# Kernel tuning notes

Measured on AMD Instinct MI355X. Metric: run time of the kernel, lower is better.

The kernel has to match this reference:

```python
import jax, jax.numpy as jnp
import numpy as np
from jax import lax

N, HW = 64, 240
C0, C1, C2, C3 = 3, 32, 64, 128
HEAD = 1280


def _conv(x, w, stride, pad):
    return lax.conv_general_dilated(
        x, w, (stride, stride), [(pad, pad), (pad, pad)],
        dimension_numbers=("NCHW", "OIHW", "NCHW"))


def _cbr(x, w, alpha, beta, stride, pad, do_relu=True):
    # conv2d with pre-folded BN: y = conv(x,w)*alpha + beta, then ReLU
    y = _conv(x, w, stride, pad)
    y = y * alpha[None, :, None, None] + beta[None, :, None, None]
    return jnp.maximum(y, 0.0) if do_relu else y


def setup_inputs() -> dict:
    key = jax.random.key(0)
    ks = jax.random.split(key, 13)
    f32 = jnp.float32
    inp = {
        "x": jax.random.normal(ks[0], (N, C0, HW, HW), dtype=f32),
        # stem 3x3 s2: 3 -> 32
        "w_stem": jax.random.normal(ks[1], (C1, C0, 3, 3), dtype=f32) * 0.1,
        "a_stem": jax.random.uniform(ks[2], (C1,), dtype=f32, minval=0.5, maxval=1.5),
        "b_stem": jax.random.normal(ks[3], (C1,), dtype=f32) * 0.1,
        # mid 3x3 s2: 32 -> 64
        "w1": jax.random.normal(ks[4], (C2, C1, 3, 3), dtype=f32) * 0.05,
        "a1": jax.random.uniform(ks[5], (C2,), dtype=f32, minval=0.5, maxval=1.5),
        "b1": jax.random.normal(ks[6], (C2,), dtype=f32) * 0.1,
        # pointwise 1x1 s1: 64 -> 128
        "w2": jax.random.normal(ks[7], (C3, C2, 1, 1), dtype=f32) * 0.05,
        "a2": jax.random.uniform(ks[8], (C3,), dtype=f32, minval=0.5, maxval=1.5),
        "b2": jax.random.normal(ks[9], (C3,), dtype=f32) * 0.1,
        # head: GAP + GEMV (w2d [Cout, Cin]) + BN-fold + ReLU
        "w_head": jax.random.normal(ks[10], (HEAD, C3), dtype=f32) * 0.05,
        "a_head": jax.random.uniform(ks[11], (HEAD,), dtype=f32, minval=0.5, maxval=1.5),
        "b_head": jax.random.normal(ks[12], (HEAD,), dtype=f32) * 0.1,
    }
    return inp


def reference(x, w_stem, a_stem, b_stem, w1, a1, b1, w2, a2, b2,
              w_head, a_head, b_head):
    h = _cbr(x, w_stem, a_stem, b_stem, stride=2, pad=1)   # [N,32,120,120]
    h = _cbr(h, w1, a1, b1, stride=2, pad=1)               # [N,64,60,60]
    h = _cbr(h, w2, a2, b2, stride=1, pad=0)               # [N,128,60,60]
    # head: global average pool + GEMV + folded-BN affine + ReLU
    gap = h.mean(axis=(2, 3))                              # [N,128]
    out = jnp.einsum("nc,oc->no", gap, w_head)             # [N,1280]
    out = out * a_head[None, :] + b_head[None, :]
    return jnp.maximum(out, 0.0)
```

## Files before the change

kernel.cpp:

```cpp
#include <hip/hip_runtime.h>

#define N_    64
#define HW_   240
#define H1_   120
#define H2_   60
#define C0_   3
#define C1_   32
#define C2_   64
#define C3_   128
#define HEAD_ 1280

typedef unsigned short US;
typedef short bf16x8 __attribute__((ext_vector_type(8)));
typedef float f32x16 __attribute__((ext_vector_type(16)));

__device__ __forceinline__ US f2bf(float f) {
  union { float f; unsigned u; } v; v.f = f;
  unsigned r = v.u + 0x7FFF + ((v.u >> 16) & 1);
  return (US)(r >> 16);
}

#define H1Q_ROW 3968
#define H1Q_PL  1984

#define ZCHN   368
#define ZTOT   (64 * ZCHN * 4)
__global__ __launch_bounds__(256) void k0_prep(
    const float* __restrict__ w1, const float* __restrict__ w2,
    const float* __restrict__ w0,
    US* __restrict__ h1q, US* __restrict__ wt1, US* __restrict__ wt2,
    US* __restrict__ wt0, float* __restrict__ gap) {
  int gid = blockIdx.x * 256 + threadIdx.x;
  if (gid < ZTOT) {
    int c = gid >> 2, q = gid & 3;
    int n = c / ZCHN, cc = c % ZCHN;
    long off; int y;
    if (cc < 124)      { y = 0;   off = (long)cc * 32; }
    else if (cc < 248) { y = 121; off = (long)(cc - 124) * 32; }
    else               { y = cc - 247; off = H1Q_PL; }
    uint4 z; z.x = z.y = z.z = z.w = 0u;
    *(uint4*)(h1q + ((long)(n * 122 + y)) * H1Q_ROW + off + q * 8) = z;
  } else if (gid < ZTOT + 18432) {
    int e = gid - ZTOT;
    int oc = e / 288, ic = (e / 9) % 32, ky = (e / 3) % 3, kx = e % 3;
    wt1[((ky * 3 + kx) * 64 + oc) * 32 + ic] = f2bf(w1[e]);
  } else if (gid < ZTOT + 18432 + 8192) {
    int e = gid - (ZTOT + 18432);
    wt2[e] = f2bf(w2[e]);
  } else if (gid < ZTOT + 18432 + 8192 + 1024) {
    int e = gid - (ZTOT + 18432 + 8192);
    int oc = e >> 5, k = e & 31;
    wt0[e] = (k < 27) ? f2bf(w0[oc * 27 + k]) : (US)0;
  } else if (gid < ZTOT + 18432 + 8192 + 1024 + 8192) {
    gap[gid - (ZTOT + 18432 + 8192 + 1024)] = 0.f;
  }
}

#define XSW 248
__global__ __launch_bounds__(256) void k1_mfma(
    const float* __restrict__ x, const US* __restrict__ wt0,
    const float* __restrict__ alpha, const float* __restrict__ beta,
    US* __restrict__ h1q) {
  __shared__ float xs[3 * 3 * XSW];
  __shared__ US ot[128 * 32];
  int y = blockIdx.x, n = blockIdx.y;
  int iy0 = 2 * y - 1;
  const float* xn = x + (long)n * C0_ * HW_ * HW_;
  for (int e = threadIdx.x; e < 540; e += 256) {
    int m = e % 60, seg = e / 60;
    int ic = seg / 3, r = seg % 3;
    int iy = iy0 + r;
    float4 v; v.x = v.y = v.z = v.w = 0.f;
    if (iy >= 0) v = *(const float4*)(xn + (long)ic * HW_ * HW_ + iy * HW_ + 4 * m);
    *(float4*)(xs + seg * XSW + 4 + 4 * m) = v;
  }
  if (threadIdx.x < 18) {
    int seg = threadIdx.x >> 1, end = threadIdx.x & 1;
    float4 z; z.x = z.y = z.z = z.w = 0.f;
    *(float4*)(xs + seg * XSW + (end ? 244 : 0)) = z;
  }
  __syncthreads();

  int t = threadIdx.x, wv = t >> 6, l = t & 63;
  int lane31 = l & 31, half = l >> 5;
  int ox = wv * 32 + lane31;
  int oxc = ox < H1_ ? ox : (H1_ - 1);

  float fa[16];
#pragma unroll
  for (int m = 0; m < 2; m++)
#pragma unroll
    for (int j = 0; j < 8; j++) {
      int k = m * 16 + half * 8 + j;
      float v = 0.f;
      if (k < 27) {
        int ic = k / 9, rem = k - ic * 9;
        int ky = rem / 3, kx = rem - ky * 3;
        v = xs[(ic * 3 + ky) * XSW + 3 + 2 * oxc + kx];
      }
      fa[m * 8 + j] = v;
    }
  bf16x8 a0, a1;
#pragma unroll
  for (int j = 0; j < 8; j++) {
    a0[j] = (short)f2bf(fa[j]);
    a1[j] = (short)f2bf(fa[8 + j]);
  }
  const US* wb = wt0 + lane31 * 32 + half * 8;
  bf16x8 b0 = *(const bf16x8*)(wb);
  bf16x8 b1 = *(const bf16x8*)(wb + 16);

  f32x16 acc;
#pragma unroll
  for (int i = 0; i < 16; i++) acc[i] = 0.f;
  acc = __builtin_amdgcn_mfma_f32_32x32x16_bf16(a0, b0, acc, 0, 0, 0);
  acc = __builtin_amdgcn_mfma_f32_32x32x16_bf16(a1, b1, acc, 0, 0, 0);

  int oc = lane31;
  float al = alpha[oc], be = beta[oc];
#pragma unroll
  for (int r = 0; r < 16; r++) {
    int row = (r & 3) + 8 * (r >> 2) + 4 * half;
    float v = fmaxf(fmaf(acc[r], al, be), 0.f);
    ot[(wv * 32 + row) * 32 + oc] = f2bf(v);
  }
  __syncthreads();

  long rowb = ((long)(n * 122 + y + 1)) * H1Q_ROW;
  for (int u = t; u < 480; u += 256) {
    int px = u >> 2, q = u & 3;
    int pl = px & 1;
    int m = (px + 1) >> 1;
    long addr = rowb + (pl ? H1Q_PL : 0) + (long)m * 32 + q * 8;
    *(uint4*)(h1q + addr) = *(const uint4*)(ot + px * 32 + q * 8);
  }
}

#define TS 72
__device__ __forceinline__ void gld_lds16(const void* g, void* l) {
  __builtin_amdgcn_global_load_lds(
      (const __attribute__((address_space(1))) unsigned int*)g,
      (__attribute__((address_space(3))) unsigned int*)l, 16, 0, 0);
}

__global__ __launch_bounds__(256) void k2_fused(
    const US* __restrict__ h1q, const US* __restrict__ wt1,
    const US* __restrict__ wt2,
    const float* __restrict__ a1, const float* __restrict__ b1,
    const float* __restrict__ a2, const float* __restrict__ b2,
    float* __restrict__ gap) {
  __shared__ __align__(16) US st[1536 * 8];
  __shared__ __align__(16) US tile[64 * TS];
  int t = threadIdx.x, w = t >> 6, l = t & 63;
  int lane31 = l & 31, half = l >> 5;

  int flat = blockIdx.y * 60 + blockIdx.x;
  int sf = (flat & 7) * 480 + (flat >> 3);
  int n = sf / 60, y = sf - n * 60;

  const US* src = h1q + ((long)(n * 122 + 2 * y)) * H1Q_ROW;
#pragma unroll
  for (int i = 0; i < 6; i++) {
    int b = (i * 256 + t) * 16;
    int sb = b ^ (((b >> 7) & 7) << 4);
    gld_lds16((const char*)src + sb, (char*)st + b);
  }
  __syncthreads();

  int wm = w & 1, wn = w >> 1;
  int px = wm * 32 + lane31;
  int xx = px < 60 ? px : 59;
  int oc = wn * 32 + lane31;
  int abase = xx * 32 + half * 8;

  f32x16 acc;
#pragma unroll
  for (int i = 0; i < 16; i++) acc[i] = 0.f;

#pragma unroll
  for (int ky = 0; ky < 3; ky++) {
#pragma unroll
    for (int kx = 0; kx < 3; kx++) {
      int aoff = ky * 3968 + (kx == 1 ? 0 : (kx == 0 ? 1984 : 2016)) + abase;
      const US* wk = wt1 + ((ky * 3 + kx) * 64 + oc) * 32 + half * 8;
#pragma unroll
      for (int c = 0; c < 2; c++) {
        int u = aoff + c * 16;
        int us = u ^ (((u >> 6) & 7) << 3);
        bf16x8 av = *(const bf16x8*)(st + us);
        bf16x8 bv = *(const bf16x8*)(wk + c * 16);
        acc = __builtin_amdgcn_mfma_f32_32x32x16_bf16(av, bv, acc, 0, 0, 0);
      }
    }
  }
  {
    float al = a1[oc], be = b1[oc];
#pragma unroll
    for (int r = 0; r < 16; r++) {
      int row = (r & 3) + 8 * (r >> 2) + 4 * half;
      tile[(wm * 32 + row) * TS + oc] = f2bf(fmaxf(fmaf(acc[r], al, be), 0.f));
    }
  }
  __syncthreads();

  int pt = w & 1;
  int og = w >> 1;
  const US* ab = tile + (pt * 32 + lane31) * TS + half * 8;
  bf16x8 af[4];
#pragma unroll
  for (int c = 0; c < 4; c++) af[c] = *(const bf16x8*)(ab + c * 16);

#pragma unroll
  for (int nt = 0; nt < 2; nt++) {
    int oc2 = (og * 2 + nt) * 32 + lane31;
    const US* bb = wt2 + oc2 * 64 + half * 8;
    f32x16 acc2;
#pragma unroll
    for (int i = 0; i < 16; i++) acc2[i] = 0.f;
#pragma unroll
    for (int c = 0; c < 4; c++) {
      bf16x8 bv = *(const bf16x8*)(bb + c * 16);
      acc2 = __builtin_amdgcn_mfma_f32_32x32x16_bf16(af[c], bv, acc2, 0, 0, 0);
    }
    float al2 = a2[oc2], be2 = b2[oc2];
    float s = 0.f;
    if (pt == 0) {
#pragma unroll
      for (int r = 0; r < 16; r++) s += fmaxf(fmaf(acc2[r], al2, be2), 0.f);
    } else {
#pragma unroll
      for (int r = 0; r < 16; r++) {
        int row = (r & 3) + 8 * (r >> 2) + 4 * half;
        if (32 + row < 60) s += fmaxf(fmaf(acc2[r], al2, be2), 0.f);
      }
    }
    s += __shfl_xor(s, 32);
    if (half == 0) atomicAdd(gap + n * C3_ + oc2, s);
  }
}

__global__ __launch_bounds__(256) void k4_head(
    const float* __restrict__ gap, const float* __restrict__ wh,
    const float* __restrict__ alpha, const float* __restrict__ beta,
    float* __restrict__ out) {
  __shared__ float g[C3_];
  int n = blockIdx.y;
  int o = blockIdx.x * 256 + threadIdx.x;
  if (threadIdx.x < C3_)
    g[threadIdx.x] = gap[n * C3_ + threadIdx.x] * (1.f / 3600.f);
  __syncthreads();
  const float* wr = wh + (long)o * C3_;
  float acc = 0.f;
#pragma unroll 8
  for (int c = 0; c < C3_; c += 4) {
    float4 wv = *(const float4*)(wr + c);
    acc = fmaf(wv.x, g[c],     acc);
    acc = fmaf(wv.y, g[c + 1], acc);
    acc = fmaf(wv.z, g[c + 2], acc);
    acc = fmaf(wv.w, g[c + 3], acc);
  }
  out[n * HEAD_ + o] = fmaxf(fmaf(acc, alpha[o], beta[o]), 0.f);
}

extern "C" void kernel_launch(void* const* d_in, const int* in_sizes, int n_in,
                              void* d_out, int out_size, void* d_ws,
                              size_t ws_size, hipStream_t stream) {
  const float* x      = (const float*)d_in[0];
  const float* w_stem = (const float*)d_in[1];
  const float* a_stem = (const float*)d_in[2];
  const float* b_stem = (const float*)d_in[3];
  const float* w1     = (const float*)d_in[4];
  const float* a1     = (const float*)d_in[5];
  const float* b1     = (const float*)d_in[6];
  const float* w2     = (const float*)d_in[7];
  const float* a2     = (const float*)d_in[8];
  const float* b2     = (const float*)d_in[9];
  const float* wh     = (const float*)d_in[10];
  const float* ah     = (const float*)d_in[11];
  const float* bh     = (const float*)d_in[12];
  float* out = (float*)d_out;

  US* h1q = (US*)d_ws;
  US* wt1 = h1q + (size_t)N_ * 122 * H1Q_ROW;
  US* wt2 = wt1 + 9 * 64 * 32;
  US* wt0 = wt2 + C3_ * C2_;
  float* gap = (float*)(wt0 + 1024);

  {
    int total = ZTOT + 18432 + 8192 + 1024 + 8192;
    k0_prep<<<(total + 255) / 256, 256, 0, stream>>>(w1, w2, w_stem, h1q,
                                                     wt1, wt2, wt0, gap);
  }
  {
    dim3 grid(H1_, N_);
    k1_mfma<<<grid, 256, 0, stream>>>(x, wt0, a_stem, b_stem, h1q);
  }
  {
    dim3 grid(H2_, N_);
    k2_fused<<<grid, 256, 0, stream>>>(h1q, wt1, wt2, a1, b1, a2, b2, gap);
  }
  {
    dim3 grid(HEAD_ / 256, N_);
    k4_head<<<grid, 256, 0, stream>>>(gap, wh, ah, bh, out);
  }
}
```

Baseline: 169.2 us.

## Make k2 blocks loop over output rows with ring-buffered input rows and register-resident weights

The fused conv kernel now gives each block a strip of 7-8 output rows of one image instead of a single row. Input rows sit in a 6-row LDS ring buffer that is prefetched asynchronously one step ahead, so the two overlapping rows between consecutive outputs are reused. Both conv weight sets and the BN constants are loaded into registers once per block, and launch bounds request two blocks per CU. The head kernel now handles 8 images per block to reuse each weight row. The trade-off is a much smaller k2 grid (512 blocks), higher register pressure and two extra barriers per row.

```diff
diff --git a/kernel.cpp b/kernel.cpp
--- a/kernel.cpp
+++ b/kernel.cpp
@@ -143,99 +143,137 @@
       (__attribute__((address_space(3))) unsigned int*)l, 16, 0, 0);
 }
 
-__global__ __launch_bounds__(256) void k2_fused(
+__global__ __launch_bounds__(256, 2) void k2_fused(
     const US* __restrict__ h1q, const US* __restrict__ wt1,
     const US* __restrict__ wt2,
     const float* __restrict__ a1, const float* __restrict__ b1,
     const float* __restrict__ a2, const float* __restrict__ b2,
     float* __restrict__ gap) {
-  __shared__ __align__(16) US st[1536 * 8];
+  __shared__ __align__(16) US st[6 * 4096];
   __shared__ __align__(16) US tile[64 * TS];
   int t = threadIdx.x, w = t >> 6, l = t & 63;
   int lane31 = l & 31, half = l >> 5;
 
-  int flat = blockIdx.y * 60 + blockIdx.x;
-  int sf = (flat & 7) * 480 + (flat >> 3);
-  int n = sf / 60, y = sf - n * 60;
-
-  const US* src = h1q + ((long)(n * 122 + 2 * y)) * H1Q_ROW;
-#pragma unroll
-  for (int i = 0; i < 6; i++) {
-    int b = (i * 256 + t) * 16;
-    int sb = b ^ (((b >> 7) & 7) << 4);
-    gld_lds16((const char*)src + sb, (char*)st + b);
-  }
-  __syncthreads();
+  int n = 8 * blockIdx.x + (blockIdx.y & 7);
+  int bxr = blockIdx.y >> 3;
+  int ny = bxr < 4 ? 8 : 7;
+  int y0 = bxr < 4 ? bxr * 8 : 32 + (bxr - 4) * 7;
+
+  const char* nb = (const char*)(h1q + (long)(n * 122) * H1Q_ROW);
 
   int wm = w & 1, wn = w >> 1;
+  int oc = wn * 32 + lane31;
+  int pt = w & 1, og = w >> 1;
+  bf16x8 wA[9][2];
+#pragma unroll
+  for (int kk = 0; kk < 9; kk++)
+#pragma unroll
+    for (int c = 0; c < 2; c++)
+      wA[kk][c] = *(const bf16x8*)(wt1 + (kk * 64 + oc) * 32 + half * 8 + c * 16);
+  bf16x8 wB[2][4];
+  float al2[2], be2[2];
+#pragma unroll
+  for (int nt = 0; nt < 2; nt++) {
+    int oc2 = (og * 2 + nt) * 32 + lane31;
+#pragma unroll
+    for (int c = 0; c < 4; c++)
+      wB[nt][c] = *(const bf16x8*)(wt2 + oc2 * 64 + half * 8 + c * 16);
+    al2[nt] = a2[oc2]; be2[nt] = b2[oc2];
+  }
+  float al1 = a1[oc], be1 = b1[oc];
+
   int px = wm * 32 + lane31;
   int xx = px < 60 ? px : 59;
-  int oc = wn * 32 + lane31;
   int abase = xx * 32 + half * 8;
-
-  f32x16 acc;
-#pragma unroll
-  for (int i = 0; i < 16; i++) acc[i] = 0.f;
-
-#pragma unroll
-  for (int ky = 0; ky < 3; ky++) {
-#pragma unroll
-    for (int kx = 0; kx < 3; kx++) {
-      int aoff = ky * 3968 + (kx == 1 ? 0 : (kx == 0 ? 1984 : 2016)) + abase;
-      const US* wk = wt1 + ((ky * 3 + kx) * 64 + oc) * 32 + half * 8;
-#pragma unroll
-      for (int c = 0; c < 2; c++) {
-        int u = aoff + c * 16;
-        int us = u ^ (((u >> 6) & 7) << 3);
-        bf16x8 av = *(const bf16x8*)(st + us);
-        bf16x8 bv = *(const bf16x8*)(wk + c * 16);
-        acc = __builtin_amdgcn_mfma_f32_32x32x16_bf16(av, bv, acc, 0, 0, 0);
+  int usofs[3][2];
+#pragma unroll
+  for (int kx = 0; kx < 3; kx++)
+#pragma unroll
+    for (int c = 0; c < 2; c++) {
+      int uo = (kx == 1 ? 0 : (kx == 0 ? 1984 : 2016)) + abase + c * 16;
+      usofs[kx][c] = uo ^ (((uo >> 6) & 7) << 3);
+    }
+
+#pragma unroll
+  for (int i = 0; i < 6; i++) {
+    int c = i * 256 + t;
+    int rw = c >> 9;
+    int b = (c & 511) * 16;
+    int sb = b ^ (((b >> 7) & 7) << 4);
+    int r = 2 * y0 + rw;
+    gld_lds16(nb + (long)r * 7936 + sb, (char*)st + (r % 6) * 8192 + b);
+  }
+  __syncthreads();
+
+  for (int iy = 0; iy < ny; iy++) {
+    int y = y0 + iy;
+    if (iy + 1 < ny) {
+#pragma unroll
+      for (int i = 0; i < 4; i++) {
+        int c = i * 256 + t;
+        int rw = c >> 9;
+        int b = (c & 511) * 16;
+        int sb = b ^ (((b >> 7) & 7) << 4);
+        int r = 2 * y + 3 + rw;
+        gld_lds16(nb + (long)r * 7936 + sb,
+                  (char*)st + (r % 6) * 8192 + b);
       }
     }
-  }
-  {
-    float al = a1[oc], be = b1[oc];
+
+    f32x16 acc;
+#pragma unroll
+    for (int i = 0; i < 16; i++) acc[i] = 0.f;
+#pragma unroll
+    for (int ky = 0; ky < 3; ky++) {
+      int r = 2 * y + ky;
+      int sb6 = (r % 6) * 4096;
+#pragma unroll
+      for (int kx = 0; kx < 3; kx++) {
+#pragma unroll
+        for (int c = 0; c < 2; c++) {
+          bf16x8 av = *(const bf16x8*)(st + sb6 + usofs[kx][c]);
+          acc = __builtin_amdgcn_mfma_f32_32x32x16_bf16(av, wA[ky * 3 + kx][c],
+                                                        acc, 0, 0, 0);
+        }
+      }
+    }
 #pragma unroll
     for (int r = 0; r < 16; r++) {
       int row = (r & 3) + 8 * (r >> 2) + 4 * half;
-      tile[(wm * 32 + row) * TS + oc] = f2bf(fmaxf(fmaf(acc[r], al, be), 0.f));
-    }
-  }
-  __syncthreads();
-
-  int pt = w & 1;
-  int og = w >> 1;
-  const US* ab = tile + (pt * 32 + lane31) * TS + half * 8;
-  bf16x8 af[4];
-#pragma unroll
-  for (int c = 0; c < 4; c++) af[c] = *(const bf16x8*)(ab + c * 16);
-
-#pragma unroll
-  for (int nt = 0; nt < 2; nt++) {
-    int oc2 = (og * 2 + nt) * 32 + lane31;
-    const US* bb = wt2 + oc2 * 64 + half * 8;
-    f32x16 acc2;
-#pragma unroll
-    for (int i = 0; i < 16; i++) acc2[i] = 0.f;
-#pragma unroll
-    for (int c = 0; c < 4; c++) {
-      bf16x8 bv = *(const bf16x8*)(bb + c * 16);
-      acc2 = __builtin_amdgcn_mfma_f32_32x32x16_bf16(af[c], bv, acc2, 0, 0, 0);
-    }
-    float al2 = a2[oc2], be2 = b2[oc2];
-    float s = 0.f;
-    if (pt == 0) {
-#pragma unroll
-      for (int r = 0; r < 16; r++) s += fmaxf(fmaf(acc2[r], al2, be2), 0.f);
-    } else {
-#pragma unroll
-      for (int r = 0; r < 16; r++) {
-        int row = (r & 3) + 8 * (r >> 2) + 4 * half;
-        if (32 + row < 60) s += fmaxf(fmaf(acc2[r], al2, be2), 0.f);
+      tile[(wm * 32 + row) * TS + oc] = f2bf(fmaxf(fmaf(acc[r], al1, be1), 0.f));
+    }
+    __syncthreads();
+
+    const US* ab = tile + (pt * 32 + lane31) * TS + half * 8;
+    bf16x8 af[4];
+#pragma unroll
+    for (int c = 0; c < 4; c++) af[c] = *(const bf16x8*)(ab + c * 16);
+
+#pragma unroll
+    for (int nt = 0; nt < 2; nt++) {
+      int oc2 = (og * 2 + nt) * 32 + lane31;
+      f32x16 acc2;
+#pragma unroll
+      for (int i = 0; i < 16; i++) acc2[i] = 0.f;
+#pragma unroll
+      for (int c = 0; c < 4; c++)
+        acc2 = __builtin_amdgcn_mfma_f32_32x32x16_bf16(af[c], wB[nt][c], acc2,
+                                                       0, 0, 0);
+      float s = 0.f;
+      if (pt == 0) {
+#pragma unroll
+        for (int r = 0; r < 16; r++) s += fmaxf(fmaf(acc2[r], al2[nt], be2[nt]), 0.f);
+      } else {
+#pragma unroll
+        for (int r = 0; r < 16; r++) {
+          int row = (r & 3) + 8 * (r >> 2) + 4 * half;
+          if (32 + row < 60) s += fmaxf(fmaf(acc2[r], al2[nt], be2[nt]), 0.f);
+        }
       }
-    }
-    s += __shfl_xor(s, 32);
-    if (half == 0) atomicAdd(gap + n * C3_ + oc2, s);
+      s += __shfl_xor(s, 32);
+      if (half == 0) atomicAdd(gap + n * C3_ + oc2, s);
+    }
+    __syncthreads();
   }
 }
 
@@ -243,23 +281,33 @@
     const float* __restrict__ gap, const float* __restrict__ wh,
     const float* __restrict__ alpha, const float* __restrict__ beta,
     float* __restrict__ out) {
-  __shared__ float g[C3_];
-  int n = blockIdx.y;
-  int o = blockIdx.x * 256 + threadIdx.x;
-  if (threadIdx.x < C3_)
-    g[threadIdx.x] = gap[n * C3_ + threadIdx.x] * (1.f / 3600.f);
+  __shared__ float g[8 * C3_];
+  int n0 = blockIdx.y * 8;
+  int t = threadIdx.x;
+  for (int e = t; e < 8 * C3_; e += 256)
+    g[e] = gap[n0 * C3_ + e] * (1.f / 3600.f);
   __syncthreads();
+  int o = blockIdx.x * 256 + t;
   const float* wr = wh + (long)o * C3_;
-  float acc = 0.f;
-#pragma unroll 8
+  float acc[8];
+#pragma unroll
+  for (int i = 0; i < 8; i++) acc[i] = 0.f;
+#pragma unroll 4
   for (int c = 0; c < C3_; c += 4) {
     float4 wv = *(const float4*)(wr + c);
-    acc = fmaf(wv.x, g[c],     acc);
-    acc = fmaf(wv.y, g[c + 1], acc);
-    acc = fmaf(wv.z, g[c + 2], acc);
-    acc = fmaf(wv.w, g[c + 3], acc);
-  }
-  out[n * HEAD_ + o] = fmaxf(fmaf(acc, alpha[o], beta[o]), 0.f);
+#pragma unroll
+    for (int i = 0; i < 8; i++) {
+      const float* gi = g + i * C3_ + c;
+      acc[i] = fmaf(wv.x, gi[0], acc[i]);
+      acc[i] = fmaf(wv.y, gi[1], acc[i]);
+      acc[i] = fmaf(wv.z, gi[2], acc[i]);
+      acc[i] = fmaf(wv.w, gi[3], acc[i]);
+    }
+  }
+  float al = alpha[o], be = beta[o];
+#pragma unroll
+  for (int i = 0; i < 8; i++)
+    out[(n0 + i) * HEAD_ + o] = fmaxf(fmaf(acc[i], al, be), 0.f);
 }
 
 extern "C" void kernel_launch(void* const* d_in, const int* in_sizes, int n_in,
@@ -296,11 +344,11 @@
     k1_mfma<<<grid, 256, 0, stream>>>(x, wt0, a_stem, b_stem, h1q);
   }
   {
-    dim3 grid(H2_, N_);
+    dim3 grid(8, N_);
     k2_fused<<<grid, 256, 0, stream>>>(h1q, wt1, wt2, a1, b1, a2, b2, gap);
   }
   {
-    dim3 grid(HEAD_ / 256, N_);
+    dim3 grid(HEAD_ / 256, 8);
     k4_head<<<grid, 256, 0, stream>>>(gap, wh, ah, bh, out);
   }
 }
```

New measurement: 153.0 us. 1.11x faster.
